# Kernel optimization log

Hardware: AMD Instinct MI355X
Metric: run time of the kernel (lower is better)

## Reference

```python
import jax, jax.numpy as jnp
import numpy as np

# Inner-product factors for Cl(1,3) (Minkowski metric diag(+,-,-,-)).
# For blade e_b, <~e_b e_b>_0 = product of the metric signs of its constituent vectors.
# Blade order: [1, e0,e1,e2,e3, e01,e02,e03,e12,e13,e23, e012,e013,e023,e123, e0123]
_IPF = jnp.array([1, 1, -1, -1, -1, -1, -1, -1, 1, 1, 1, 1, 1, 1, -1, -1], dtype=jnp.float32)

B, H, N, CMV, CS = 4, 8, 2048, 8, 16


def setup_inputs() -> dict:
    key = jax.random.key(0)
    ks = jax.random.split(key, 6)
    f = lambda k, s: jax.random.normal(k, s, dtype=jnp.float32)
    return {
        "q_mv": f(ks[0], (B, H, N, CMV, 16)),
        "k_mv": f(ks[1], (B, H, N, CMV, 16)),
        "v_mv": f(ks[2], (B, H, N, CMV, 16)),
        "q_s": f(ks[3], (B, H, N, CS)),
        "k_s": f(ks[4], (B, H, N, CS)),
        "v_s": f(ks[5], (B, H, N, CS)),
    }


def reference(q_mv, k_mv, v_mv, q_s, k_s, v_s):
    b, h, n, cmv, _ = q_mv.shape
    cs = q_s.shape[-1]
    cmv_out = v_mv.shape[-2]
    cs_out = v_s.shape[-1]
    # GA inner product on mv part = euclidean dot after applying metric factors to queries
    q = jnp.concatenate([(q_mv * _IPF).reshape(b, h, n, cmv * 16), q_s], axis=-1)
    k = jnp.concatenate([k_mv.reshape(b, h, n, cmv * 16), k_s], axis=-1)
    v = jnp.concatenate([v_mv.reshape(b, h, n, cmv_out * 16), v_s], axis=-1)
    scale = 1.0 / np.sqrt(q.shape[-1]).astype(np.float32)  # torch SDPA default scale
    scores = jnp.einsum("bhid,bhjd->bhij", q, k) * scale  # [B,H,N,N]
    attn = jax.nn.softmax(scores, axis=-1)
    out = jnp.einsum("bhij,bhjd->bhid", attn, v)
    out_mv = out[..., : cmv_out * 16].reshape(b, h, n, cmv_out, 16)
    out_s = out[..., cmv_out * 16 : cmv_out * 16 + cs_out]
    return out_mv, out_s
```

## Files before the change

### kernel.cpp

```cpp
#include <hip/hip_runtime.h>
#include <cstdint>
#include <math.h>


#define BH    32
#define N_    2048
#define DMV   128
#define DS    16
#define D_    144
#define BM    256
#define BN    64
#define NKIT  (N_ / BN)
#define KSTR  152
#define VSTR  72
#define KCHUNKS (BN * KSTR / 8)
#define VCHUNKS (D_ * VSTR / 8)
#define KP_BYTES ((size_t)BH * N_ * KSTR * 2)
#define QSCALE 0.12022458674074693f
#define TSTR  156

typedef __bf16 bf16_8 __attribute__((ext_vector_type(8)));
typedef __bf16 bf16_4 __attribute__((ext_vector_type(4)));
typedef __bf16 bf16_2 __attribute__((ext_vector_type(2)));
typedef float  f32x4  __attribute__((ext_vector_type(4)));
typedef float  f32x16 __attribute__((ext_vector_type(16)));

#define GLOAD_LDS16(g, l)                                                     \
  __builtin_amdgcn_global_load_lds(                                           \
      (const __attribute__((address_space(1))) void*)(g),                     \
      (__attribute__((address_space(3))) void*)(l), 16, 0, 0)

__device__ __forceinline__ f32x16 mfma32(bf16_8 a, bf16_8 b, f32x16 c) {
  return __builtin_amdgcn_mfma_f32_32x32x16_bf16(a, b, c, 0, 0, 0);
}

__device__ __forceinline__ bf16_4 cvt4(f32x4 x) {
  bf16_4 w; w[0]=(__bf16)x[0]; w[1]=(__bf16)x[1]; w[2]=(__bf16)x[2]; w[3]=(__bf16)x[3];
  return w;
}

__global__ __launch_bounds__(256)
void pack_k(const float* __restrict__ kmv, const float* __restrict__ ks_,
            __bf16* __restrict__ kp) {
  const unsigned g = blockIdx.x * 256u + threadIdx.x;
  const unsigned row = g / 19u, seg = g - row * 19u;
  bf16_8 o;
  if (seg < 16) {
    const f32x4* p = (const f32x4*)(kmv + (size_t)row * DMV + seg * 8);
    f32x4 a = p[0], bb = p[1];
#pragma unroll
    for (int j = 0; j < 8; ++j) o[j] = (__bf16)((j < 4) ? a[j] : bb[j - 4]);
  } else if (seg < 18) {
    const f32x4* p = (const f32x4*)(ks_ + (size_t)row * DS + (seg - 16) * 8);
    f32x4 a = p[0], bb = p[1];
#pragma unroll
    for (int j = 0; j < 8; ++j) o[j] = (__bf16)((j < 4) ? a[j] : bb[j - 4]);
  } else {
#pragma unroll
    for (int j = 0; j < 8; ++j) o[j] = (__bf16)0.0f;
  }
  *(bf16_8*)(kp + (size_t)row * KSTR + seg * 8) = o;
}

__global__ __launch_bounds__(256)
void pack_vt(const float* __restrict__ vmv, const float* __restrict__ vs,
             __bf16* __restrict__ vt) {
  __shared__ __align__(16) __bf16 sT[64 * TSTR];
  const int tile = blockIdx.x;
  const int t = threadIdx.x;
  const int n = t >> 2, c = t & 3;
  const float* mv = vmv + (size_t)(tile * 64 + n) * DMV;
  const float* sv = vs  + (size_t)(tile * 64 + n) * DS;
  __bf16* row = &sT[n * TSTR];
  if (c < 3) {
#pragma unroll
    for (int i = 0; i < 9; ++i)
      *(bf16_4*)&row[c * 36 + 4 * i] = cvt4(*(const f32x4*)(mv + c * 36 + 4 * i));
  } else {
#pragma unroll
    for (int i = 0; i < 5; ++i)
      *(bf16_4*)&row[108 + 4 * i] = cvt4(*(const f32x4*)(mv + 108 + 4 * i));
#pragma unroll
    for (int i = 0; i < 4; ++i)
      *(bf16_4*)&row[128 + 4 * i] = cvt4(*(const f32x4*)(sv + 4 * i));
  }
  __syncthreads();
  __bf16* vtt = vt + (size_t)tile * (D_ * VSTR);
#pragma unroll
  for (int k = 0; k < 18; ++k) {
    int idx = t + 256 * k;
    int d = idx >> 5, j = idx & 31;
    bf16_2 p; p[0] = sT[(2 * j) * TSTR + d]; p[1] = sT[(2 * j + 1) * TSTR + d];
    *(bf16_2*)&vtt[d * VSTR + 2 * j] = p;
  }
}

__device__ __forceinline__ bf16_8 load_q_frag(const float* qmv_row, const float* qs_row, int k0) {
  bf16_8 f;
  if (k0 < DMV) {
    const f32x4* p = (const f32x4*)(qmv_row + k0);
    f32x4 a = p[0], b = p[1];
    int hi8 = k0 & 8;
#pragma unroll
    for (int j = 0; j < 8; ++j) {
      float v = (j < 4) ? a[j] : b[j - 4];
      bool pos = hi8 ? (j < 6) : (j < 2);
      f[j] = (__bf16)(v * (pos ? QSCALE : -QSCALE));
    }
  } else {
    const f32x4* p = (const f32x4*)(qs_row + (k0 - DMV));
    f32x4 a = p[0], b = p[1];
#pragma unroll
    for (int j = 0; j < 8; ++j) {
      float v = (j < 4) ? a[j] : b[j - 4];
      f[j] = (__bf16)(v * QSCALE);
    }
  }
  return f;
}

__global__ __launch_bounds__(512, 2)
void geo_attn_kernel(const float* __restrict__ q_mv, const float* __restrict__ q_s,
                     const __bf16* __restrict__ kp, const __bf16* __restrict__ vt,
                     float* __restrict__ out)
{
  __shared__ __align__(16) __bf16 sVT[3][D_ * VSTR];
  __shared__ __align__(16) __bf16 sK[2][BN * KSTR];

  const int tid  = threadIdx.x;
  const int lane = tid & 63;
  const int w    = tid >> 6;
  const int role = (w >> 2) & 1;
  const int c32  = lane & 31;
  const int hi   = lane >> 5;
  const int flat = blockIdx.x;
  const int xcd  = flat & 7;
  const int jj   = flat >> 3;
  const int bh   = xcd * 4 + (jj & 3);
  const int qb   = jj >> 2;
  const int qbase = qb * BM;
  const size_t bh_n = (size_t)bh * N_;

  bf16_8 qf[9];
  {
    const int mrow = qbase + w * 32 + c32;
    const float* qmv_row = q_mv + (bh_n + mrow) * DMV;
    const float* qs_row  = q_s  + (bh_n + mrow) * DS;
#pragma unroll
    for (int ks = 0; ks < 9; ++ks)
      qf[ks] = load_q_frag(qmv_row, qs_row, ks * 16 + hi * 8);
  }

  f32x16 of[5];
#pragma unroll
  for (int dt = 0; dt < 5; ++dt)
#pragma unroll
    for (int r = 0; r < 16; ++r) of[dt][r] = 0.0f;
  float m_i = -INFINITY, l_i = 0.0f;

  const __bf16* kbase = kp + bh_n * KSTR;
  const __bf16* vbase = vt + (size_t)bh * NKIT * (D_ * VSTR);

  auto stage = [&](int it) {
    const __bf16* kt = kbase + (size_t)(it * BN) * KSTR;
    __bf16* dK = &sK[it & 1][0];
    GLOAD_LDS16(kt + tid * 8, dK + tid * 8);
    GLOAD_LDS16(kt + (tid + 512) * 8, dK + (tid + 512) * 8);
    if (tid < KCHUNKS - 1024)
      GLOAD_LDS16(kt + (tid + 1024) * 8, dK + (tid + 1024) * 8);
    const __bf16* vtt = vbase + (size_t)it * (D_ * VSTR);
    __bf16* dV = &sVT[it % 3][0];
    GLOAD_LDS16(vtt + tid * 8, dV + tid * 8);
    GLOAD_LDS16(vtt + (tid + 512) * 8, dV + (tid + 512) * 8);
    if (tid < VCHUNKS - 1024)
      GLOAD_LDS16(vtt + (tid + 1024) * 8, dV + (tid + 1024) * 8);
  };

  f32x16 sf[2];
  auto qk = [&](int t) {
    const __bf16* sKt = &sK[t & 1][0];
#pragma unroll
    for (int nt = 0; nt < 2; ++nt)
#pragma unroll
      for (int r = 0; r < 16; ++r) sf[nt][r] = 0.0f;
    __builtin_amdgcn_s_setprio(1);
#pragma unroll
    for (int ks = 0; ks < 9; ++ks) {
      bf16_8 kb0 = *(const bf16_8*)&sKt[(c32)      * KSTR + ks * 16 + hi * 8];
      bf16_8 kb1 = *(const bf16_8*)&sKt[(32 + c32) * KSTR + ks * 16 + hi * 8];
      sf[0] = mfma32(kb0, qf[ks], sf[0]);
      sf[1] = mfma32(kb1, qf[ks], sf[1]);
    }
    __builtin_amdgcn_s_setprio(0);
  };

  auto sm = [&]() {
    float al = 1.0f, m_use;
    float a[8];
#pragma unroll
    for (int r = 0; r < 8; ++r)
      a[r] = fmaxf(fmaxf(sf[0][r], sf[0][r + 8]), fmaxf(sf[1][r], sf[1][r + 8]));
    float mx = fmaxf(fmaxf(fmaxf(a[0], a[1]), fmaxf(a[2], a[3])),
                     fmaxf(fmaxf(a[4], a[5]), fmaxf(a[6], a[7])));
    mx = fmaxf(mx, __shfl_xor(mx, 32));

    if (__all(mx <= m_i + 8.0f)) {
      m_use = m_i;
    } else {
      float mnew = fmaxf(m_i, mx);
      al = __builtin_amdgcn_exp2f(m_i - mnew);
      m_i = mnew; m_use = mnew;
#pragma unroll
      for (int r = 0; r < 16; ++r) {
        float aa = __shfl(al, (r & 3) + 8 * (r >> 2) + 4 * hi);
#pragma unroll
        for (int dt = 0; dt < 5; ++dt) of[dt][r] *= aa;
      }
    }
#pragma unroll
    for (int nt = 0; nt < 2; ++nt)
#pragma unroll
      for (int r = 0; r < 16; ++r)
        sf[nt][r] = __builtin_amdgcn_exp2f(sf[nt][r] - m_use);
    float s8[8];
#pragma unroll
    for (int r = 0; r < 8; ++r)
      s8[r] = (sf[0][r] + sf[0][r + 8]) + (sf[1][r] + sf[1][r + 8]);
    float rs = ((s8[0] + s8[1]) + (s8[2] + s8[3])) + ((s8[4] + s8[5]) + (s8[6] + s8[7]));
    rs += __shfl_xor(rs, 32);
    l_i = l_i * al + rs;
  };

  auto pv = [&](int t) {
    const __bf16* sV = &sVT[t % 3][0];
#pragma unroll
    for (int ks = 0; ks < 4; ++ks) {
      const int nt = ks >> 1;
      const int Ra = 8 * (ks & 1);
      unsigned x0, x1, y0, y1;
      asm("v_cvt_pk_bf16_f32 %0, %1, %2" : "=v"(x0) : "v"(sf[nt][Ra + 0]), "v"(sf[nt][Ra + 1]));
      asm("v_cvt_pk_bf16_f32 %0, %1, %2" : "=v"(x1) : "v"(sf[nt][Ra + 2]), "v"(sf[nt][Ra + 3]));
      asm("v_cvt_pk_bf16_f32 %0, %1, %2" : "=v"(y0) : "v"(sf[nt][Ra + 4]), "v"(sf[nt][Ra + 5]));
      asm("v_cvt_pk_bf16_f32 %0, %1, %2" : "=v"(y1) : "v"(sf[nt][Ra + 6]), "v"(sf[nt][Ra + 7]));
      auto s0 = __builtin_amdgcn_permlane32_swap(x0, y0, false, false);
      auto s1 = __builtin_amdgcn_permlane32_swap(x1, y1, false, false);
      union { unsigned u[4]; bf16_8 v; } pu;
      pu.u[0] = s0[0]; pu.u[1] = s1[0]; pu.u[2] = s0[1]; pu.u[3] = s1[1];
      __builtin_amdgcn_s_setprio(1);
#pragma unroll
      for (int dt = 0; dt < 5; ++dt) {
        bf16_8 vb = *(const bf16_8*)&sV[(dt * 32 + c32) * VSTR + ks * 16 + hi * 8];
        of[dt] = mfma32(pu.v, vb, of[dt]);
      }
      __builtin_amdgcn_s_setprio(0);
    }
  };

  stage(0);
  __syncthreads();

  for (int t = 0; t < NKIT; ++t) {
    if (t + 1 < NKIT) stage(t + 1);
    if (role == 0) {
      qk(t); sm(); pv(t);
    } else {
      if (t > 0) { sm(); pv(t - 1); }
      qk(t);
    }
    __syncthreads();
  }
  if (role == 1) { sm(); pv(NKIT - 1); }

  float* out_mv = out;
  float* out_s  = out + (size_t)BH * N_ * DMV;
#pragma unroll
  for (int r = 0; r < 16; ++r) {
    const int ml  = (r & 3) + 8 * (r >> 2) + 4 * hi;
    const float linv = __builtin_amdgcn_rcpf(__shfl(l_i, ml));
    const int row = qbase + w * 32 + ml;
#pragma unroll
    for (int dt = 0; dt < 4; ++dt)
      out_mv[(bh_n + row) * DMV + dt * 32 + c32] = of[dt][r] * linv;
    if (c32 < DS)
      out_s[(bh_n + row) * DS + c32] = of[4][r] * linv;
  }
}

extern "C" void kernel_launch(void* const* d_in, const int* in_sizes, int n_in,
                              void* d_out, int out_size, void* d_ws, size_t ws_size,
                              hipStream_t stream) {
  (void)in_sizes; (void)n_in; (void)out_size; (void)ws_size;
  const float* q_mv = (const float*)d_in[0];
  const float* k_mv = (const float*)d_in[1];
  const float* v_mv = (const float*)d_in[2];
  const float* q_s  = (const float*)d_in[3];
  const float* k_s  = (const float*)d_in[4];
  const float* v_s  = (const float*)d_in[5];
  float* out = (float*)d_out;

  __bf16* kp = (__bf16*)d_ws;
  __bf16* vt = (__bf16*)((char*)d_ws + KP_BYTES);

  pack_k<<<(BH * N_ * 19) / 256, 256, 0, stream>>>(k_mv, k_s, kp);
  pack_vt<<<BH * NKIT, 256, 0, stream>>>(v_mv, v_s, vt);

  geo_attn_kernel<<<dim3(256), 512, 0, stream>>>(q_mv, q_s, kp, vt, out);
}
```

Measured before the change: 241.7 us.

## Merge K/V staging into double buffer with prefetch distance two and vmcnt waits

Replaces the separate double-buffered K and triple-buffered V shared arrays with one combined double buffer holding K and V per tile. Loads are issued two tiles ahead and completion is tracked with explicit vmcnt waits plus raw barriers. The ping-pong role split, where half the waves deferred softmax and PV to the next iteration, is removed so all waves run QK, softmax and PV in order. This aims to hide global-load latency more deeply and cut synchronisation overhead, but it drops the intra-block overlap between MFMA and softmax work that the role split provided.

```diff
diff --git a/kernel.cpp b/kernel.cpp
--- a/kernel.cpp
+++ b/kernel.cpp
@@ -13,11 +13,14 @@
 #define NKIT  (N_ / BN)
 #define KSTR  152
 #define VSTR  72
-#define KCHUNKS (BN * KSTR / 8)
-#define VCHUNKS (D_ * VSTR / 8)
 #define KP_BYTES ((size_t)BH * N_ * KSTR * 2)
 #define QSCALE 0.12022458674074693f
 #define TSTR  156
+#define CK    1216
+#define CV    2656
+#define CTOT  2688
+#define BUFE  (CTOT * 8)
+#define VOFF  (CK * 8)
 
 typedef __bf16 bf16_8 __attribute__((ext_vector_type(8)));
 typedef __bf16 bf16_4 __attribute__((ext_vector_type(4)));
@@ -124,13 +127,11 @@
                      const __bf16* __restrict__ kp, const __bf16* __restrict__ vt,
                      float* __restrict__ out)
 {
-  __shared__ __align__(16) __bf16 sVT[3][D_ * VSTR];
-  __shared__ __align__(16) __bf16 sK[2][BN * KSTR];
+  __shared__ __align__(16) __bf16 sbuf[2][BUFE];
 
   const int tid  = threadIdx.x;
   const int lane = tid & 63;
   const int w    = tid >> 6;
-  const int role = (w >> 2) & 1;
   const int c32  = lane & 31;
   const int hi   = lane >> 5;
   const int flat = blockIdx.x;
@@ -161,24 +162,37 @@
   const __bf16* kbase = kp + bh_n * KSTR;
   const __bf16* vbase = vt + (size_t)bh * NKIT * (D_ * VSTR);
 
-  auto stage = [&](int it) {
-    const __bf16* kt = kbase + (size_t)(it * BN) * KSTR;
-    __bf16* dK = &sK[it & 1][0];
-    GLOAD_LDS16(kt + tid * 8, dK + tid * 8);
-    GLOAD_LDS16(kt + (tid + 512) * 8, dK + (tid + 512) * 8);
-    if (tid < KCHUNKS - 1024)
-      GLOAD_LDS16(kt + (tid + 1024) * 8, dK + (tid + 1024) * 8);
+  auto stage = [&](int it, int bu) {
+    const __bf16* kt  = kbase + (size_t)(it * BN) * KSTR;
     const __bf16* vtt = vbase + (size_t)it * (D_ * VSTR);
-    __bf16* dV = &sVT[it % 3][0];
-    GLOAD_LDS16(vtt + tid * 8, dV + tid * 8);
-    GLOAD_LDS16(vtt + (tid + 512) * 8, dV + (tid + 512) * 8);
-    if (tid < VCHUNKS - 1024)
-      GLOAD_LDS16(vtt + (tid + 1024) * 8, dV + (tid + 1024) * 8);
+    if (w < 6) {
+#pragma unroll
+      for (int s = 0; s < 5; ++s) {
+        int c = w * 320 + s * 64 + lane;
+        const __bf16* src;
+        if (c < CK) src = kt + c * 8;
+        else { int vc = c - CK; if (vc >= 1296) vc -= 1296; src = vtt + vc * 8; }
+        GLOAD_LDS16(src, &sbuf[bu][c * 8]);
+      }
+    } else {
+#pragma unroll
+      for (int s = 0; s < 6; ++s) {
+        int c = 1920 + (w - 6) * 384 + s * 64 + lane;
+        const __bf16* src;
+        if (c < CK) src = kt + c * 8;
+        else { int vc = c - CK; if (vc >= 1296) vc -= 1296; src = vtt + vc * 8; }
+        GLOAD_LDS16(src, &sbuf[bu][c * 8]);
+      }
+    }
+  };
+  auto wait_prev_stage = [&]() {
+    if (w < 6) asm volatile("s_waitcnt vmcnt(5)" ::: "memory");
+    else       asm volatile("s_waitcnt vmcnt(6)" ::: "memory");
   };
 
   f32x16 sf[2];
-  auto qk = [&](int t) {
-    const __bf16* sKt = &sK[t & 1][0];
+  auto qk = [&](int bu) {
+    const __bf16* sKt = &sbuf[bu][0];
 #pragma unroll
     for (int nt = 0; nt < 2; ++nt)
 #pragma unroll
@@ -231,8 +245,8 @@
     l_i = l_i * al + rs;
   };
 
-  auto pv = [&](int t) {
-    const __bf16* sV = &sVT[t % 3][0];
+  auto pv = [&](int bu) {
+    const __bf16* sV = &sbuf[bu][VOFF];
 #pragma unroll
     for (int ks = 0; ks < 4; ++ks) {
       const int nt = ks >> 1;
@@ -256,20 +270,25 @@
     }
   };
 
-  stage(0);
-  __syncthreads();
+  stage(0, 0);
+  stage(1, 1);
+  wait_prev_stage();
+  __builtin_amdgcn_s_barrier();
 
   for (int t = 0; t < NKIT; ++t) {
-    if (t + 1 < NKIT) stage(t + 1);
-    if (role == 0) {
-      qk(t); sm(); pv(t);
+    const int cur = t & 1;
+    qk(cur); sm(); pv(cur);
+
+    asm volatile("s_waitcnt lgkmcnt(0)" ::: "memory");
+    __builtin_amdgcn_s_barrier();
+    if (t + 2 < NKIT) {
+      stage(t + 2, cur);
+      wait_prev_stage();
     } else {
-      if (t > 0) { sm(); pv(t - 1); }
-      qk(t);
-    }
-    __syncthreads();
-  }
-  if (role == 1) { sm(); pv(NKIT - 1); }
+      asm volatile("s_waitcnt vmcnt(0)" ::: "memory");
+    }
+    __builtin_amdgcn_s_barrier();
+  }
 
   float* out_mv = out;
   float* out_s  = out + (size_t)BH * N_ * DMV;
```

Result: no change. 241.7 us (+0.0%).
